# Optimization experiments

Measured on AMD Instinct MI355X. Metric: run time of the kernel, lower is better.

## Reference

```python
import jax, jax.numpy as jnp
import numpy as np

D_MODEL = 1024
N_HEADS = 16
D_K = D_MODEL // N_HEADS


def setup_inputs() -> dict:
    key = jax.random.key(0)
    k1, k2, k3 = jax.random.split(key, 3)
    x = jax.random.normal(k1, (4, 2048, D_MODEL), dtype=jnp.float32)
    # torch nn.Linear(d, 3d, bias=False): y = x @ W.T ; we store W.T directly as (in, out)
    w_qkv = jax.random.normal(k2, (D_MODEL, 3 * D_MODEL), dtype=jnp.float32) * (1.0 / np.sqrt(D_MODEL))
    w_out = jax.random.normal(k3, (D_MODEL, D_MODEL), dtype=jnp.float32) * (1.0 / np.sqrt(D_MODEL))
    return {"x": x, "w_qkv": w_qkv, "w_out": w_out}


def reference(x, w_qkv, w_out):
    B, T, D = x.shape
    qkv = jnp.einsum('btd,de->bte', x, w_qkv)  # (B,T,3D)
    q, k, v = jnp.split(qkv, 3, axis=-1)
    # split heads -> (B,H,T,d_k)
    def split_heads(t):
        return t.reshape(B, T, N_HEADS, D_K).transpose(0, 2, 1, 3)
    q, k, v = split_heads(q), split_heads(k), split_heads(v)
    scale = 1.0 / np.sqrt(D_K).astype(np.float32)
    scores = jnp.einsum('bhqd,bhkd->bhqk', q, k) * scale  # (B,H,T,T)
    causal = jnp.triu(jnp.full((T, T), -jnp.inf, dtype=scores.dtype), k=1)
    scores = scores + causal[None, None]
    weights = jax.nn.softmax(scores, axis=-1)
    attn = jnp.einsum('bhqk,bhkd->bhqd', weights, v)
    attn = attn.transpose(0, 2, 1, 3).reshape(B, T, D)
    return jnp.einsum('btd,de->bte', attn, w_out)
```

## Files before the change

### kernel.cpp

```cpp
#include <hip/hip_runtime.h>
#include <hip/hip_bf16.h>

typedef short short8 __attribute__((ext_vector_type(8)));
typedef float f32x4 __attribute__((ext_vector_type(4)));

#define MFMA16(a, b, c) __builtin_amdgcn_mfma_f32_16x16x32_bf16((a), (b), (c), 0, 0, 0)

#define GLOAD16(gp, lp)                                                    \
    __builtin_amdgcn_global_load_lds(                                      \
        (const __attribute__((address_space(1))) unsigned int*)(gp),       \
        (__attribute__((address_space(3))) unsigned int*)(lp), 16, 0, 0)

__device__ __forceinline__ unsigned short f2b(float x) {
    unsigned int u = __float_as_uint(x);
    unsigned int r = u + 0x7FFFu + ((u >> 16) & 1u);
    return (unsigned short)(r >> 16);
}

#if __has_builtin(__builtin_amdgcn_cvt_pk_bf16_f32)
__device__ __forceinline__ unsigned pack2(float a, float b) {
    auto v = __builtin_amdgcn_cvt_pk_bf16_f32(a, b);
    unsigned u;
    __builtin_memcpy(&u, &v, 4);
    return u;
}
#else
__device__ __forceinline__ unsigned pack2(float a, float b) {
    return (unsigned)f2b(a) | ((unsigned)f2b(b) << 16);
}
#endif

__global__ __launch_bounds__(256) void cast4_kernel(const float* __restrict__ in,
                                                    unsigned short* __restrict__ out,
                                                    int n4) {
    int i = blockIdx.x * 256 + threadIdx.x;
    if (i < n4) {
        float4 v = ((const float4*)in)[i];
        ushort4 o;
        o.x = f2b(v.x); o.y = f2b(v.y); o.z = f2b(v.z); o.w = f2b(v.w);
        ((ushort4*)out)[i] = o;
    }
}

__global__ __launch_bounds__(256) void transpose_cast_f32(const float* __restrict__ in,
                                                          unsigned short* __restrict__ out,
                                                          int K, int N) {
    __shared__ unsigned short Ls[64 * 66];
    const int k0 = blockIdx.y * 64, n0 = blockIdx.x * 64;
    const int tid = threadIdx.x;
    const int krow = tid >> 4, nc4 = (tid & 15) * 4;
#pragma unroll
    for (int p = 0; p < 4; p++) {
        float4 v = *(const float4*)(in + (size_t)(k0 + krow + p * 16) * N + n0 + nc4);
        unsigned* d32 = (unsigned*)(Ls + (krow + p * 16) * 66 + nc4);
        d32[0] = pack2(v.x, v.y);
        d32[1] = pack2(v.z, v.w);
    }
    __syncthreads();
    const int n = tid >> 3, kc = (tid & 7) * 8;
#pragma unroll
    for (int p = 0; p < 2; p++) {
        int nn = n + p * 32;
        unsigned short w[8];
#pragma unroll
        for (int j = 0; j < 8; j++) w[j] = Ls[(kc + j) * 66 + nn];
        *(short8*)(out + (size_t)(n0 + nn) * K + k0 + kc) = *(short8*)w;
    }
}

__global__ __launch_bounds__(256) void vt_transpose(const unsigned short* __restrict__ qkv,
                                                    unsigned short* __restrict__ Vt) {
    const int T = 2048, E = 3072;
    __shared__ unsigned short Ls[64 * 66];
    const int b = blockIdx.z, h = blockIdx.y, t0 = blockIdx.x * 64;
    const int tid = threadIdx.x;
    const int trow = tid >> 3, dc = (tid & 7) * 8;
    const unsigned short* src = qkv + (size_t)(b * T + t0) * E + 2048 + h * 64;
#pragma unroll
    for (int p = 0; p < 2; p++) {
        short8 v = *(const short8*)(src + (size_t)(trow + p * 32) * E + dc);
        unsigned tmp[4];
        *(short8*)tmp = v;
        unsigned* d32 = (unsigned*)(Ls + (trow + p * 32) * 66 + dc);
        d32[0] = tmp[0]; d32[1] = tmp[1]; d32[2] = tmp[2]; d32[3] = tmp[3];
    }
    __syncthreads();
    const int d = tid >> 3, tc = (tid & 7) * 8;
    const size_t obase = ((size_t)(b * 16 + h) * 64) * 2048;
#pragma unroll
    for (int p = 0; p < 2; p++) {
        int dd = d + p * 32;
        unsigned short w[8];
#pragma unroll
        for (int j = 0; j < 8; j++) w[j] = Ls[(tc + j) * 66 + dd];
        *(short8*)(Vt + obase + (size_t)dd * 2048 + t0 + tc) = *(short8*)w;
    }
}

template <bool WRITE_BF16, bool SCALE_Q>
__global__ __launch_bounds__(256) void gemm_nt(const unsigned short* __restrict__ A,
                                               const unsigned short* __restrict__ Bt,
                                               void* __restrict__ C,
                                               int M, int N, int K, int lda) {
    __shared__ unsigned short As[128 * 32];
    __shared__ unsigned short Bs[128 * 32];

    const int tid  = threadIdx.x;
    const int wave = tid >> 6;
    const int lane = tid & 63;
    const int l16  = lane & 15;
    const int quad = lane >> 4;
    const int m0 = blockIdx.y * 128;
    const int n0 = blockIdx.x * 128;
    const int wm = (wave >> 1) * 64;
    const int wn = (wave & 1) * 64;

    const int srow = lane >> 2;
    const int scol = (lane & 3) * 8;
    const unsigned short* Ag0 = A  + (size_t)(m0 + wave * 32 + srow)      * lda + scol;
    const unsigned short* Ag1 = A  + (size_t)(m0 + wave * 32 + 16 + srow) * lda + scol;
    const unsigned short* Bg0 = Bt + (size_t)(n0 + wave * 32 + srow)      * K + scol;
    const unsigned short* Bg1 = Bt + (size_t)(n0 + wave * 32 + 16 + srow) * K + scol;
    unsigned short* Al0 = As + (wave * 2 + 0) * 512;
    unsigned short* Al1 = As + (wave * 2 + 1) * 512;
    unsigned short* Bl0 = Bs + (wave * 2 + 0) * 512;
    unsigned short* Bl1 = Bs + (wave * 2 + 1) * 512;

    f32x4 acc[4][4] = {};

    for (int k0 = 0; k0 < K; k0 += 32) {
        __syncthreads();
        GLOAD16(Ag0 + k0, Al0);
        GLOAD16(Ag1 + k0, Al1);
        GLOAD16(Bg0 + k0, Bl0);
        GLOAD16(Bg1 + k0, Bl1);
        __syncthreads();

        short8 af[4], bf[4];
#pragma unroll
        for (int i = 0; i < 4; i++) {
            af[i] = *(const short8*)(As + (wm + i * 16 + l16) * 32 + quad * 8);
            bf[i] = *(const short8*)(Bs + (wn + i * 16 + l16) * 32 + quad * 8);
        }
#pragma unroll
        for (int i = 0; i < 4; i++)
#pragma unroll
            for (int j = 0; j < 4; j++)
                acc[i][j] = MFMA16(af[i], bf[j], acc[i][j]);
    }

    const float QSCALE = 0.125f * 1.44269504f;
#pragma unroll
    for (int i = 0; i < 4; i++)
#pragma unroll
        for (int j = 0; j < 4; j++)
#pragma unroll
            for (int r = 0; r < 4; r++) {
                int row = m0 + wm + i * 16 + quad * 4 + r;
                int col = n0 + wn + j * 16 + l16;
                float v = acc[i][j][r];
                if (SCALE_Q && col < 1024) v *= QSCALE;
                if (WRITE_BF16)
                    ((unsigned short*)C)[(size_t)row * N + col] = f2b(v);
                else
                    ((float*)C)[(size_t)row * N + col] = v;
            }
}

__global__ __launch_bounds__(256) void attention_kernel(const unsigned short* qkv,
                                                        const unsigned short* Vt,
                                                        unsigned short* attn) {
    const int T = 2048, E = 3072;
    const int b = blockIdx.z, h = blockIdx.y;
    const int qs = blockIdx.x;
    int qq = (b & 2) ? ((qs + 8) & 15) : qs;
    const int qb = (b & 1) ? (15 - qq) : qq;
    const int qb0 = qb * 128;
    const int tid = threadIdx.x, wave = tid >> 6, lane = tid & 63;
    const int l16 = lane & 15, quad = lane >> 4;
    const int qw0 = qb0 + wave * 32;

    const unsigned short* Qp  = qkv + (size_t)b * T * E + h * 64;
    const unsigned short* Kp  = Qp + 1024;
    const unsigned short* Vbh = Vt + ((size_t)(b * 16 + h) * 64) * 2048;

    __shared__ unsigned short Ks[64 * 72];
    __shared__ unsigned short Vts[64 * 72];
    __shared__ unsigned short Ps[4][32 * 40];
    unsigned short* Psw = Ps[wave];

    short8 qf[2][2];
#pragma unroll
    for (int nt = 0; nt < 2; nt++)
#pragma unroll
        for (int kd = 0; kd < 2; kd++)
            qf[nt][kd] = *(const short8*)(Qp + (size_t)(qw0 + nt * 16 + l16) * E + kd * 32 + quad * 8);

    f32x4 o[4][2] = {};
    float l_acc[2] = {0.f, 0.f};

    const int srow = tid >> 2, sch = (tid & 3) * 8;

    const int nkt = qb0 / 64 + 2;
    for (int kt = 0; kt < nkt; kt++) {
        const int tk0 = kt * 64;
        short8 kv0 = *(const short8*)(Kp + (size_t)(tk0 + srow) * E + sch);
        short8 kv1 = *(const short8*)(Kp + (size_t)(tk0 + srow) * E + 32 + sch);
        short8 vv0 = *(const short8*)(Vbh + (size_t)srow * T + tk0 + sch);
        short8 vv1 = *(const short8*)(Vbh + (size_t)srow * T + tk0 + 32 + sch);
        __syncthreads();
        *(short8*)(Ks + srow * 72 + sch)       = kv0;
        *(short8*)(Ks + srow * 72 + 32 + sch)  = kv1;
        *(short8*)(Vts + srow * 72 + sch)      = vv0;
        *(short8*)(Vts + srow * 72 + 32 + sch) = vv1;
        __syncthreads();

#pragma unroll
        for (int th = 0; th < 2; th++) {
            if (tk0 + th * 32 > qw0 + 31) continue;

            f32x4 s[2][2] = {};
#pragma unroll
            for (int mi = 0; mi < 2; mi++) {
                const int mt = th * 2 + mi;
                short8 kf0 = *(const short8*)(Ks + (mt * 16 + l16) * 72 + quad * 8);
                short8 kf1 = *(const short8*)(Ks + (mt * 16 + l16) * 72 + 32 + quad * 8);
#pragma unroll
                for (int nt = 0; nt < 2; nt++)
                    if (tk0 + mt * 16 <= qw0 + nt * 16 + 15) {
                        s[nt][mi] = MFMA16(kf0, qf[nt][0], s[nt][mi]);
                        s[nt][mi] = MFMA16(kf1, qf[nt][1], s[nt][mi]);
                    }
            }
#pragma unroll
            for (int nt = 0; nt < 2; nt++)
#pragma unroll
                for (int mi = 0; mi < 2; mi++) {
                    const int mt = th * 2 + mi;
                    unsigned pk0 = 0, pk1 = 0;
                    if (tk0 + mt * 16 <= qw0 + nt * 16 + 15) {
                        const bool full = (tk0 + mt * 16 + 15) <= (qw0 + nt * 16);
                        float p[4];
#pragma unroll
                        for (int r = 0; r < 4; r++) {
                            float e = __builtin_amdgcn_exp2f(s[nt][mi][r]);
                            if (!full)
                                e = (tk0 + mt * 16 + quad * 4 + r <= qw0 + nt * 16 + l16) ? e : 0.f;
                            p[r] = e;
                        }
                        l_acc[nt] += (p[0] + p[1]) + (p[2] + p[3]);
                        pk0 = pack2(p[0], p[1]);
                        pk1 = pack2(p[2], p[3]);
                    }
                    uint2 pr; pr.x = pk0; pr.y = pk1;
                    *(uint2*)(Psw + (nt * 16 + l16) * 40 + mi * 16 + quad * 4) = pr;
                }
            short8 vf[4];
#pragma unroll
            for (int dt = 0; dt < 4; dt++)
                vf[dt] = *(const short8*)(Vts + (dt * 16 + l16) * 72 + th * 32 + quad * 8);
#pragma unroll
            for (int nt = 0; nt < 2; nt++) {
                if (tk0 + th * 32 > qw0 + nt * 16 + 15) continue;
                short8 pf = *(const short8*)(Psw + (nt * 16 + l16) * 40 + quad * 8);
#pragma unroll
                for (int dt = 0; dt < 4; dt++)
                    o[dt][nt] = MFMA16(vf[dt], pf, o[dt][nt]);
            }
        }
    }

    float rl[2];
#pragma unroll
    for (int nt = 0; nt < 2; nt++) {
        float l = l_acc[nt];
        l += __shfl_xor(l, 16);
        l += __shfl_xor(l, 32);
        rl[nt] = 1.f / l;
    }
#pragma unroll
    for (int nt = 0; nt < 2; nt++) {
        const int q = qw0 + nt * 16 + l16;
#pragma unroll
        for (int dt = 0; dt < 4; dt++) {
            ushort4 wv;
            wv.x = f2b(o[dt][nt][0] * rl[nt]);
            wv.y = f2b(o[dt][nt][1] * rl[nt]);
            wv.z = f2b(o[dt][nt][2] * rl[nt]);
            wv.w = f2b(o[dt][nt][3] * rl[nt]);
            *(ushort4*)(attn + (size_t)(b * T + q) * E + h * 64 + dt * 16 + quad * 4) = wv;
        }
    }
}

extern "C" void kernel_launch(void* const* d_in, const int* in_sizes, int n_in,
                              void* d_out, int out_size, void* d_ws, size_t ws_size,
                              hipStream_t stream) {
    const float* x     = (const float*)d_in[0];
    const float* w_qkv = (const float*)d_in[1];
    const float* w_out = (const float*)d_in[2];
    float* out = (float*)d_out;

    const int M = 8192, D = 1024, E = 3072;

    char* ws = (char*)d_ws;
    unsigned short* xb    = (unsigned short*)ws;
    unsigned short* wqkvT = (unsigned short*)(ws + (size_t)16777216);
    unsigned short* woutT = (unsigned short*)(ws + (size_t)23068672);
    unsigned short* qkvb  = (unsigned short*)(ws + (size_t)25165824);
    unsigned short* Vt    = xb;

    cast4_kernel<<<M * D / 4 / 256, 256, 0, stream>>>(x, xb, M * D / 4);
    transpose_cast_f32<<<dim3(E / 64, D / 64), 256, 0, stream>>>(w_qkv, wqkvT, D, E);
    transpose_cast_f32<<<dim3(D / 64, D / 64), 256, 0, stream>>>(w_out, woutT, D, D);

    gemm_nt<true, true><<<dim3(E / 128, M / 128), 256, 0, stream>>>(xb, wqkvT, qkvb, M, E, D, D);

    vt_transpose<<<dim3(32, 16, 4), 256, 0, stream>>>(qkvb, Vt);

    attention_kernel<<<dim3(16, 16, 4), 256, 0, stream>>>(qkvb, Vt, qkvb + 2048);

    gemm_nt<false, false><<<dim3(D / 128, M / 128), 256, 0, stream>>>(qkvb + 2048, woutT, out, M, D, D, E);
}
```

Baseline: 293.4 us.

## Shrink attention query tiles, async-load K/V with LDS swizzle, smaller output GEMM tile

The attention kernel now uses 64-query blocks with one 16-row query tile per wave. Blocks are launched on a flat grid ordered longest-first so the causal work is balanced. K and V tiles are loaded with direct global-to-LDS loads into XOR-swizzled, unpadded buffers, replacing register staging with padded rows. The GEMM gains a templated M tile and the same swizzle to cut LDS bank conflicts; the output projection uses a 64-row tile to launch more blocks. In exchange, each attention block reuses less K/V per load and the swizzle adds index arithmetic.

```diff
diff --git a/kernel.cpp b/kernel.cpp
--- a/kernel.cpp
+++ b/kernel.cpp
@@ -97,12 +97,14 @@
     }
 }
 
-template <bool WRITE_BF16, bool SCALE_Q>
+template <int MT, bool WRITE_BF16, bool SCALE_Q>
 __global__ __launch_bounds__(256) void gemm_nt(const unsigned short* __restrict__ A,
                                                const unsigned short* __restrict__ Bt,
                                                void* __restrict__ C,
                                                int M, int N, int K, int lda) {
-    __shared__ unsigned short As[128 * 32];
+    constexpr int MI  = MT / 32;
+    constexpr int ACH = MT / 64;
+    __shared__ unsigned short As[MT * 32];
     __shared__ unsigned short Bs[128 * 32];
 
     const int tid  = threadIdx.x;
@@ -110,40 +112,47 @@
     const int lane = tid & 63;
     const int l16  = lane & 15;
     const int quad = lane >> 4;
-    const int m0 = blockIdx.y * 128;
+    const int m0 = blockIdx.y * MT;
     const int n0 = blockIdx.x * 128;
-    const int wm = (wave >> 1) * 64;
+    const int wm = (wave >> 1) * (MT / 2);
     const int wn = (wave & 1) * 64;
 
     const int srow = lane >> 2;
-    const int scol = (lane & 3) * 8;
-    const unsigned short* Ag0 = A  + (size_t)(m0 + wave * 32 + srow)      * lda + scol;
-    const unsigned short* Ag1 = A  + (size_t)(m0 + wave * 32 + 16 + srow) * lda + scol;
-    const unsigned short* Bg0 = Bt + (size_t)(n0 + wave * 32 + srow)      * K + scol;
-    const unsigned short* Bg1 = Bt + (size_t)(n0 + wave * 32 + 16 + srow) * K + scol;
-    unsigned short* Al0 = As + (wave * 2 + 0) * 512;
-    unsigned short* Al1 = As + (wave * 2 + 1) * 512;
-    unsigned short* Bl0 = Bs + (wave * 2 + 0) * 512;
-    unsigned short* Bl1 = Bs + (wave * 2 + 1) * 512;
-
-    f32x4 acc[4][4] = {};
+    const int scol = (((lane & 3) ^ ((lane >> 3) & 3)) * 8);
+    const int sw8  = ((l16 >> 1) & 3) * 8;
+
+    const unsigned short* Ag[ACH]; unsigned short* Al[ACH];
+#pragma unroll
+    for (int p = 0; p < ACH; p++) {
+        Ag[p] = A + (size_t)(m0 + (wave * ACH + p) * 16 + srow) * lda + scol;
+        Al[p] = As + (wave * ACH + p) * 512;
+    }
+    const unsigned short* Bg[2]; unsigned short* Bl[2];
+#pragma unroll
+    for (int p = 0; p < 2; p++) {
+        Bg[p] = Bt + (size_t)(n0 + (wave * 2 + p) * 16 + srow) * K + scol;
+        Bl[p] = Bs + (wave * 2 + p) * 512;
+    }
+
+    f32x4 acc[MI][4] = {};
 
     for (int k0 = 0; k0 < K; k0 += 32) {
         __syncthreads();
-        GLOAD16(Ag0 + k0, Al0);
-        GLOAD16(Ag1 + k0, Al1);
-        GLOAD16(Bg0 + k0, Bl0);
-        GLOAD16(Bg1 + k0, Bl1);
+#pragma unroll
+        for (int p = 0; p < ACH; p++) GLOAD16(Ag[p] + k0, Al[p]);
+#pragma unroll
+        for (int p = 0; p < 2; p++) GLOAD16(Bg[p] + k0, Bl[p]);
         __syncthreads();
 
-        short8 af[4], bf[4];
-#pragma unroll
-        for (int i = 0; i < 4; i++) {
-            af[i] = *(const short8*)(As + (wm + i * 16 + l16) * 32 + quad * 8);
-            bf[i] = *(const short8*)(Bs + (wn + i * 16 + l16) * 32 + quad * 8);
-        }
-#pragma unroll
-        for (int i = 0; i < 4; i++)
+        short8 af[MI], bf[4];
+#pragma unroll
+        for (int i = 0; i < MI; i++)
+            af[i] = *(const short8*)(As + (wm + i * 16 + l16) * 32 + (quad * 8 ^ sw8));
+#pragma unroll
+        for (int j = 0; j < 4; j++)
+            bf[j] = *(const short8*)(Bs + (wn + j * 16 + l16) * 32 + (quad * 8 ^ sw8));
+#pragma unroll
+        for (int i = 0; i < MI; i++)
 #pragma unroll
             for (int j = 0; j < 4; j++)
                 acc[i][j] = MFMA16(af[i], bf[j], acc[i][j]);
@@ -151,7 +160,7 @@
 
     const float QSCALE = 0.125f * 1.44269504f;
 #pragma unroll
-    for (int i = 0; i < 4; i++)
+    for (int i = 0; i < MI; i++)
 #pragma unroll
         for (int j = 0; j < 4; j++)
 #pragma unroll
@@ -171,125 +180,112 @@
                                                         const unsigned short* Vt,
                                                         unsigned short* attn) {
     const int T = 2048, E = 3072;
-    const int b = blockIdx.z, h = blockIdx.y;
-    const int qs = blockIdx.x;
-    int qq = (b & 2) ? ((qs + 8) & 15) : qs;
-    const int qb = (b & 1) ? (15 - qq) : qq;
-    const int qb0 = qb * 128;
+    const int bi = blockIdx.x;
+    const int qb = 31 - (bi >> 6);
+    const int hb = bi & 63;
+    const int b = hb >> 4, h = hb & 15;
+    const int qb0 = qb * 64;
     const int tid = threadIdx.x, wave = tid >> 6, lane = tid & 63;
     const int l16 = lane & 15, quad = lane >> 4;
-    const int qw0 = qb0 + wave * 32;
+    const int qw0 = qb0 + wave * 16;
 
     const unsigned short* Qp  = qkv + (size_t)b * T * E + h * 64;
     const unsigned short* Kp  = Qp + 1024;
     const unsigned short* Vbh = Vt + ((size_t)(b * 16 + h) * 64) * 2048;
 
-    __shared__ unsigned short Ks[64 * 72];
-    __shared__ unsigned short Vts[64 * 72];
-    __shared__ unsigned short Ps[4][32 * 40];
+    __shared__ unsigned short Ks[2][64 * 32];
+    __shared__ unsigned short Vts[2][64 * 32];
+    __shared__ unsigned short Ps[4][16 * 40];
     unsigned short* Psw = Ps[wave];
 
-    short8 qf[2][2];
-#pragma unroll
-    for (int nt = 0; nt < 2; nt++)
-#pragma unroll
-        for (int kd = 0; kd < 2; kd++)
-            qf[nt][kd] = *(const short8*)(Qp + (size_t)(qw0 + nt * 16 + l16) * E + kd * 32 + quad * 8);
-
-    f32x4 o[4][2] = {};
-    float l_acc[2] = {0.f, 0.f};
-
-    const int srow = tid >> 2, sch = (tid & 3) * 8;
-
-    const int nkt = qb0 / 64 + 2;
-    for (int kt = 0; kt < nkt; kt++) {
+    short8 qf[2];
+#pragma unroll
+    for (int kd = 0; kd < 2; kd++)
+        qf[kd] = *(const short8*)(Qp + (size_t)(qw0 + l16) * E + kd * 32 + quad * 8);
+
+    f32x4 o[4] = {};
+    float l_acc = 0.f;
+
+    const int srow = lane >> 2;
+    const int scol = (((lane & 3) ^ ((lane >> 3) & 3)) * 8);
+    const int sw8  = ((l16 >> 1) & 3) * 8;
+    const size_t ktstep = (wave < 2) ? (size_t)64 * E : (size_t)64;
+    const size_t cstep  = (wave < 2) ? (size_t)16 * E : (size_t)16 * T;
+    const unsigned short* g0 = (wave < 2)
+            ? Kp + (size_t)srow * E + wave * 32 + scol
+            : Vbh + (size_t)srow * T + (wave - 2) * 32 + scol;
+    unsigned short* l0 = (wave < 2) ? Ks[wave] : Vts[wave - 2];
+
+    for (int kt = 0; kt <= qb; kt++) {
         const int tk0 = kt * 64;
-        short8 kv0 = *(const short8*)(Kp + (size_t)(tk0 + srow) * E + sch);
-        short8 kv1 = *(const short8*)(Kp + (size_t)(tk0 + srow) * E + 32 + sch);
-        short8 vv0 = *(const short8*)(Vbh + (size_t)srow * T + tk0 + sch);
-        short8 vv1 = *(const short8*)(Vbh + (size_t)srow * T + tk0 + 32 + sch);
+        const unsigned short* g = g0 + (size_t)kt * ktstep;
         __syncthreads();
-        *(short8*)(Ks + srow * 72 + sch)       = kv0;
-        *(short8*)(Ks + srow * 72 + 32 + sch)  = kv1;
-        *(short8*)(Vts + srow * 72 + sch)      = vv0;
-        *(short8*)(Vts + srow * 72 + 32 + sch) = vv1;
+#pragma unroll
+        for (int c = 0; c < 4; c++) GLOAD16(g + c * cstep, l0 + c * 512);
         __syncthreads();
 
 #pragma unroll
         for (int th = 0; th < 2; th++) {
-            if (tk0 + th * 32 > qw0 + 31) continue;
-
-            f32x4 s[2][2] = {};
+            if (tk0 + th * 32 > qw0 + 15) continue;
+
+            f32x4 s[2];
+            bool act[2];
 #pragma unroll
             for (int mi = 0; mi < 2; mi++) {
-                const int mt = th * 2 + mi;
-                short8 kf0 = *(const short8*)(Ks + (mt * 16 + l16) * 72 + quad * 8);
-                short8 kf1 = *(const short8*)(Ks + (mt * 16 + l16) * 72 + 32 + quad * 8);
-#pragma unroll
-                for (int nt = 0; nt < 2; nt++)
-                    if (tk0 + mt * 16 <= qw0 + nt * 16 + 15) {
-                        s[nt][mi] = MFMA16(kf0, qf[nt][0], s[nt][mi]);
-                        s[nt][mi] = MFMA16(kf1, qf[nt][1], s[nt][mi]);
+                const int t0 = tk0 + (th * 2 + mi) * 16;
+                act[mi] = (t0 <= qw0 + 15);
+                s[mi] = (f32x4){0.f, 0.f, 0.f, 0.f};
+                if (act[mi]) {
+                    const int row = (th * 2 + mi) * 16 + l16;
+                    short8 kf0 = *(const short8*)(Ks[0] + row * 32 + (quad * 8 ^ sw8));
+                    short8 kf1 = *(const short8*)(Ks[1] + row * 32 + (quad * 8 ^ sw8));
+                    s[mi] = MFMA16(kf0, qf[0], s[mi]);
+                    s[mi] = MFMA16(kf1, qf[1], s[mi]);
+                }
+            }
+#pragma unroll
+            for (int mi = 0; mi < 2; mi++) {
+                const int t0 = tk0 + (th * 2 + mi) * 16;
+                unsigned pk0 = 0, pk1 = 0;
+                if (act[mi]) {
+                    const bool full = (t0 + 15) <= qw0;
+                    float p[4];
+#pragma unroll
+                    for (int r = 0; r < 4; r++) {
+                        float e = __builtin_amdgcn_exp2f(s[mi][r]);
+                        if (!full)
+                            e = (t0 + quad * 4 + r <= qw0 + l16) ? e : 0.f;
+                        p[r] = e;
                     }
+                    l_acc += (p[0] + p[1]) + (p[2] + p[3]);
+                    pk0 = pack2(p[0], p[1]);
+                    pk1 = pack2(p[2], p[3]);
+                }
+                uint2 pr; pr.x = pk0; pr.y = pk1;
+                *(uint2*)(Psw + l16 * 40 + mi * 16 + quad * 4) = pr;
             }
-#pragma unroll
-            for (int nt = 0; nt < 2; nt++)
-#pragma unroll
-                for (int mi = 0; mi < 2; mi++) {
-                    const int mt = th * 2 + mi;
-                    unsigned pk0 = 0, pk1 = 0;
-                    if (tk0 + mt * 16 <= qw0 + nt * 16 + 15) {
-                        const bool full = (tk0 + mt * 16 + 15) <= (qw0 + nt * 16);
-                        float p[4];
-#pragma unroll
-                        for (int r = 0; r < 4; r++) {
-                            float e = __builtin_amdgcn_exp2f(s[nt][mi][r]);
-                            if (!full)
-                                e = (tk0 + mt * 16 + quad * 4 + r <= qw0 + nt * 16 + l16) ? e : 0.f;
-                            p[r] = e;
-                        }
-                        l_acc[nt] += (p[0] + p[1]) + (p[2] + p[3]);
-                        pk0 = pack2(p[0], p[1]);
-                        pk1 = pack2(p[2], p[3]);
-                    }
-                    uint2 pr; pr.x = pk0; pr.y = pk1;
-                    *(uint2*)(Psw + (nt * 16 + l16) * 40 + mi * 16 + quad * 4) = pr;
-                }
-            short8 vf[4];
-#pragma unroll
-            for (int dt = 0; dt < 4; dt++)
-                vf[dt] = *(const short8*)(Vts + (dt * 16 + l16) * 72 + th * 32 + quad * 8);
-#pragma unroll
-            for (int nt = 0; nt < 2; nt++) {
-                if (tk0 + th * 32 > qw0 + nt * 16 + 15) continue;
-                short8 pf = *(const short8*)(Psw + (nt * 16 + l16) * 40 + quad * 8);
-#pragma unroll
-                for (int dt = 0; dt < 4; dt++)
-                    o[dt][nt] = MFMA16(vf[dt], pf, o[dt][nt]);
+            short8 pf = *(const short8*)(Psw + l16 * 40 + quad * 8);
+#pragma unroll
+            for (int dt = 0; dt < 4; dt++) {
+                short8 vf = *(const short8*)(Vts[th] + (dt * 16 + l16) * 32 + (quad * 8 ^ sw8));
+                o[dt] = MFMA16(vf, pf, o[dt]);
             }
         }
     }
 
-    float rl[2];
-#pragma unroll
-    for (int nt = 0; nt < 2; nt++) {
-        float l = l_acc[nt];
-        l += __shfl_xor(l, 16);
-        l += __shfl_xor(l, 32);
-        rl[nt] = 1.f / l;
-    }
-#pragma unroll
-    for (int nt = 0; nt < 2; nt++) {
-        const int q = qw0 + nt * 16 + l16;
-#pragma unroll
-        for (int dt = 0; dt < 4; dt++) {
-            ushort4 wv;
-            wv.x = f2b(o[dt][nt][0] * rl[nt]);
-            wv.y = f2b(o[dt][nt][1] * rl[nt]);
-            wv.z = f2b(o[dt][nt][2] * rl[nt]);
-            wv.w = f2b(o[dt][nt][3] * rl[nt]);
-            *(ushort4*)(attn + (size_t)(b * T + q) * E + h * 64 + dt * 16 + quad * 4) = wv;
-        }
+    float l = l_acc;
+    l += __shfl_xor(l, 16);
+    l += __shfl_xor(l, 32);
+    const float rl = 1.f / l;
+    const int q = qw0 + l16;
+#pragma unroll
+    for (int dt = 0; dt < 4; dt++) {
+        ushort4 wv;
+        wv.x = f2b(o[dt][0] * rl);
+        wv.y = f2b(o[dt][1] * rl);
+        wv.z = f2b(o[dt][2] * rl);
+        wv.w = f2b(o[dt][3] * rl);
+        *(ushort4*)(attn + (size_t)(b * T + q) * E + h * 64 + dt * 16 + quad * 4) = wv;
     }
 }
 
@@ -314,11 +310,11 @@
     transpose_cast_f32<<<dim3(E / 64, D / 64), 256, 0, stream>>>(w_qkv, wqkvT, D, E);
     transpose_cast_f32<<<dim3(D / 64, D / 64), 256, 0, stream>>>(w_out, woutT, D, D);
 
-    gemm_nt<true, true><<<dim3(E / 128, M / 128), 256, 0, stream>>>(xb, wqkvT, qkvb, M, E, D, D);
+    gemm_nt<128, true, true><<<dim3(E / 128, M / 128), 256, 0, stream>>>(xb, wqkvT, qkvb, M, E, D, D);
 
     vt_transpose<<<dim3(32, 16, 4), 256, 0, stream>>>(qkvb, Vt);
 
-    attention_kernel<<<dim3(16, 16, 4), 256, 0, stream>>>(qkvb, Vt, qkvb + 2048);
-
-    gemm_nt<false, false><<<dim3(D / 128, M / 128), 256, 0, stream>>>(qkvb + 2048, woutT, out, M, D, D, E);
-}
+    attention_kernel<<<dim3(2048), 256, 0, stream>>>(qkvb, Vt, qkvb + 2048);
+
+    gemm_nt<64, false, false><<<dim3(D / 128, M / 64), 256, 0, stream>>>(qkvb + 2048, woutT, out, M, D, D, E);
+}
```

New measurement: 283.3 us. 3.4% less time.
